# Kernel tuning notes

Hardware: AMD Instinct MI355X
Metric: run time of the kernel (lower is better)

Reference implementation:

```python
import jax, jax.numpy as jnp
import numpy as np

B, S, D, E, K = 4, 4096, 4096, 64, 8


def setup_inputs() -> dict:
    key = jax.random.key(0)
    k1, k2, k3, k4 = jax.random.split(key, 4)
    scale = 1.0 / np.sqrt(D)
    return {
        "mh_output": jax.random.normal(k1, (B, S, D), dtype=jnp.float32),
        "W_route": jax.random.normal(k2, (E, D), dtype=jnp.float32) * scale,
        "b_route": jnp.zeros((E,), dtype=jnp.float32),
        "W_noise": jax.random.normal(k3, (E, D), dtype=jnp.float32) * scale,
        "b_noise": jnp.zeros((E,), dtype=jnp.float32),
        "noise_eps": jax.random.normal(k4, (B, S, E), dtype=jnp.float32),
        "top_k": K,
    }


def reference(mh_output, W_route, b_route, W_noise, b_noise, noise_eps, top_k):
    # two skinny GEMMs: [B,S,D] x [D,E] -> [B,S,E]
    logits = jnp.einsum("bsd,ed->bse", mh_output, W_route) + b_route
    noise_logits = jnp.einsum("bsd,ed->bse", mh_output, W_noise) + b_noise
    noisy_logits = logits + noise_eps * jax.nn.softplus(noise_logits)
    # top-k selection per token over the expert dim
    _, indices = jax.lax.top_k(noisy_logits, top_k)  # [B,S,K]
    # scatter top-k logits into a -inf tensor == mask non-topk entries
    mask = jnp.any(jax.nn.one_hot(indices, noisy_logits.shape[-1], dtype=jnp.bool_), axis=-2)  # [B,S,E]
    sparse_logits = jnp.where(mask, noisy_logits, -jnp.inf)
    router_output = jax.nn.softmax(sparse_logits, axis=-1)
    return router_output, indices
```

## Files before the change

### kernel.cpp

```cpp
#include <hip/hip_runtime.h>
#include <math.h>

#define D_DIM 4096
#define E_DIM 64
#define KTOP 8
#define TAU 2e-4f
#define BM 64
#define NTS 64
#define STB 49152
#define NST 3

#define WS_LIST 1024
#define WS_IMG 66560

typedef __attribute__((ext_vector_type(8))) short bf16x8;
typedef __attribute__((ext_vector_type(4))) float f32x4;

#define MFMA(a, b, c) __builtin_amdgcn_mfma_f32_16x16x32_bf16(a, b, c, 0, 0, 0)

typedef const __attribute__((address_space(1))) void gas_void;
typedef __attribute__((address_space(3))) void las_void;
#define GLL16(src, dst) \
    __builtin_amdgcn_global_load_lds((gas_void*)(src), (las_void*)(dst), 16, 0, 0)
#define SCHED_FENCE() __builtin_amdgcn_sched_barrier(0)

__device__ inline void split8(float4 p, float4 q, bf16x8& h8, bf16x8& l8) {
    float xx[8] = {p.x, p.y, p.z, p.w, q.x, q.y, q.z, q.w};
    union { unsigned int w[4]; bf16x8 v; } H, L;
    #pragma unroll
    for (int i = 0; i < 4; ++i) {
        float a = xx[2 * i], b = xx[2 * i + 1];
        unsigned int hw;
        asm("v_cvt_pk_bf16_f32 %0, %1, %2" : "=v"(hw) : "v"(a), "v"(b));
        float ha = __uint_as_float(hw << 16);
        float hb = __uint_as_float(hw & 0xFFFF0000u);
        float ra = a - ha, rb = b - hb;
        unsigned int lw;
        asm("v_cvt_pk_bf16_f32 %0, %1, %2" : "=v"(lw) : "v"(ra), "v"(rb));
        H.w[i] = hw; L.w[i] = lw;
    }
    h8 = H.v; l8 = L.v;
}

__global__ __launch_bounds__(256)
void preconv(const float* __restrict__ Wr, const float* __restrict__ Wn,
             unsigned short* __restrict__ img, unsigned int* __restrict__ cnt)
{
    if (blockIdx.x == 0 && threadIdx.x == 0) *cnt = 0u;
    int t = blockIdx.x * 256 + threadIdx.x;
    int kt = t >> 9, rem = t & 511;
    int koff = rem >> 7, col = rem & 127;
    int k = kt * 32 + koff * 8;
    const float* base = (col < E_DIM) ? (Wr + (size_t)col * D_DIM)
                                      : (Wn + (size_t)(col - E_DIM) * D_DIM);
    float4 x0 = *(const float4*)(base + k);
    float4 x1 = *(const float4*)(base + k + 4);
    bf16x8 h8, l8;
    split8(x0, x1, h8, l8);
    size_t o = (size_t)kt * 8192 + koff * 1024 + col * 8;
    *(bf16x8*)(img + o) = h8;
    *(bf16x8*)(img + o + 4096) = l8;
}

__global__ __launch_bounds__(512)
void router_main(const float* __restrict__ mh,
                 const unsigned short* __restrict__ Wimg,
                 const float* __restrict__ br, const float* __restrict__ bn,
                 const float* __restrict__ eps,
                 float* __restrict__ out_probs, float* __restrict__ out_idx,
                 unsigned int* __restrict__ cnt, int* __restrict__ list)
{
    extern __shared__ char smem[];
    float* zs = (float*)smem;

    const int tid  = threadIdx.x;
    const int lane = tid & 63;
    const int wv   = tid >> 6;
    const int wr   = wv >> 1;
    const int wc   = wv & 1;
    const int tok0 = blockIdx.x * BM;
    const int rloc = lane & 15;
    const int koff = lane >> 4;
    const int row  = wr * 16 + rloc;

    int boff[4];
    #pragma unroll
    for (int fc = 0; fc < 4; ++fc)
        boff[fc] = koff * 1024 + (wc * 64 + fc * 16 + rloc) * 8;

    const int4* gimg = (const int4*)Wimg;
    const float* arow = mh + (size_t)(tok0 + (tid & 63)) * D_DIM;
    const int aq0 = (tid >> 6) * 4;
    const int aq1 = aq0 + 32;

    f32x4 acc[4];
    #pragma unroll
    for (int fc = 0; fc < 4; ++fc) acc[fc] = {0.f, 0.f, 0.f, 0.f};

    auto stage_issue = [&](int t) {
        char* sb = smem + (t % NST) * STB;
        const int4* gB = gimg + (size_t)t * 2048 + tid;
        int4* dB = (int4*)sb + tid;
        GLL16(gB, dB);
        GLL16(gB + 512,  dB + 512);
        GLL16(gB + 1024, dB + 1024);
        GLL16(gB + 1536, dB + 1536);
        int4* dA = (int4*)(sb + 32768) + tid;
        GLL16(arow + t * 64 + aq0, dA);
        GLL16(arow + t * 64 + aq1, dA + 512);
    };

    stage_issue(0);
    SCHED_FENCE();
    stage_issue(1);
    SCHED_FENCE();
    asm volatile("s_waitcnt vmcnt(6)" ::: "memory");
    SCHED_FENCE();
    __builtin_amdgcn_s_barrier();
    SCHED_FENCE();

    for (int kt = 0; kt < NTS; ++kt) {
        if (kt + 2 < NTS) stage_issue(kt + 2);
        SCHED_FENCE();
        {
            const char* sb = smem + (kt % NST) * STB;
            const unsigned short* Bst = (const unsigned short*)sb;
            const char* sa = sb + 32768;
            #pragma unroll
            for (int s = 0; s < 2; ++s) {
                const int kf = s * 8 + 2 * koff;
                float4 f0 = *(const float4*)(sa + (kf * 64 + row) * 16);
                float4 f1 = *(const float4*)(sa + ((kf + 1) * 64 + row) * 16);
                bf16x8 ah, al;
                split8(f0, f1, ah, al);
                const unsigned short* bb = Bst + s * 8192;
                #pragma unroll
                for (int fc = 0; fc < 4; ++fc) {
                    bf16x8 bh = *(const bf16x8*)(bb + boff[fc]);
                    bf16x8 bl = *(const bf16x8*)(bb + 4096 + boff[fc]);
                    acc[fc] = MFMA(ah, bh, acc[fc]);
                    acc[fc] = MFMA(al, bh, acc[fc]);
                    acc[fc] = MFMA(ah, bl, acc[fc]);
                }
            }
        }
        SCHED_FENCE();
        if (kt + 2 < NTS) {
            asm volatile("s_waitcnt vmcnt(6) lgkmcnt(0)" ::: "memory");
        } else {
            asm volatile("s_waitcnt vmcnt(0) lgkmcnt(0)" ::: "memory");
        }
        SCHED_FENCE();
        __builtin_amdgcn_s_barrier();
        SCHED_FENCE();
    }

    #pragma unroll
    for (int fc = 0; fc < 4; ++fc) {
        const int col = wc * 64 + fc * 16 + rloc;
        const float bias = (col < E_DIM) ? br[col] : bn[col - E_DIM];
        #pragma unroll
        for (int rg = 0; rg < 4; ++rg) {
            const int r = wr * 16 + koff * 4 + rg;
            zs[r * 132 + col] = acc[fc][rg] + bias;
        }
    }
    __syncthreads();

    {
        const int t  = tid >> 3;
        const int e0 = (tid & 7) << 3;
        const float* ep = eps + (size_t)(tok0 + t) * E_DIM + e0;
        #pragma unroll
        for (int j = 0; j < 8; ++j) {
            float zr = zs[t * 132 + e0 + j];
            float zn = zs[t * 132 + 64 + e0 + j];
            float sp = fmaxf(zn, 0.f) + log1pf(expf(-fabsf(zn)));
            zs[t * 132 + e0 + j] = zr + ep[j] * sp;
        }
    }
    __syncthreads();

    for (int tk = 0; tk < 8; ++tk) {
        int t = wv * 8 + tk;
        float v0 = zs[t * 132 + lane];
        float v  = v0;
        float m0 = 0.f, denom = 0.f, prev = 0.f, mingap = INFINITY;
        bool selected = false;
        int rankedIdx = 0;
        #pragma unroll
        for (int k = 0; k < KTOP + 1; ++k) {
            float mv = v; int mi = lane;
            #pragma unroll
            for (int off = 32; off > 0; off >>= 1) {
                float ov = __shfl_xor(mv, off);
                int   oi = __shfl_xor(mi, off);
                if (ov > mv || (ov == mv && oi < mi)) { mv = ov; mi = oi; }
            }
            if (k == 0) m0 = mv; else mingap = fminf(mingap, prev - mv);
            prev = mv;
            if (k < KTOP) {
                denom += expf(mv - m0);
                if (lane == mi) { selected = true; v = -INFINITY; }
                if (lane == k) rankedIdx = mi;
            }
        }
        float p = selected ? expf(v0 - m0) / denom : 0.f;
        size_t tg = (size_t)(tok0 + t);
        out_probs[tg * E_DIM + lane] = p;
        if (lane < KTOP) out_idx[tg * KTOP + lane] = (float)rankedIdx;
        if (mingap < TAU && lane == 0) {
            unsigned int wpos = atomicAdd(cnt, 1u);
            list[wpos] = (int)tg;
        }
    }
}

__global__ __launch_bounds__(256)
void refine_fp64(const float* __restrict__ mh,
                 const float* __restrict__ Wr, const float* __restrict__ br,
                 const float* __restrict__ Wn, const float* __restrict__ bn,
                 const float* __restrict__ eps,
                 float* __restrict__ out_probs, float* __restrict__ out_idx,
                 const unsigned int* __restrict__ cnt, const int* __restrict__ list)
{
    __shared__ double red[128];
    const unsigned int n = *cnt;
    const int tid  = threadIdx.x;
    const int lane = tid & 63;
    const int wv   = tid >> 6;

    for (unsigned int i = blockIdx.x; i < n; i += gridDim.x) {
        const int tok = list[i];
        const float* xb = mh + (size_t)tok * D_DIM;

        for (int r = 0; r < 32; ++r) {
            const int rrow = wv * 32 + r;
            const float* wp = (rrow < E_DIM) ? (Wr + (size_t)rrow * D_DIM)
                                             : (Wn + (size_t)(rrow - E_DIM) * D_DIM);
            double s0 = 0.0, s1 = 0.0, s2 = 0.0, s3 = 0.0;
            #pragma unroll 4
            for (int k = lane * 4; k < D_DIM; k += 256) {
                float4 xv = *(const float4*)(xb + k);
                float4 w4 = *(const float4*)(wp + k);
                s0 += (double)xv.x * (double)w4.x;
                s1 += (double)xv.y * (double)w4.y;
                s2 += (double)xv.z * (double)w4.z;
                s3 += (double)xv.w * (double)w4.w;
            }
            double s = (s0 + s1) + (s2 + s3);
            #pragma unroll
            for (int off = 32; off > 0; off >>= 1) s += __shfl_xor(s, off);
            if (lane == 0) red[rrow] = s;
        }
        __syncthreads();

        if (wv == 0) {
            double zr = red[lane] + (double)br[lane];
            double zn = red[E_DIM + lane] + (double)bn[lane];
            double sp = fmax(zn, 0.0) + log1p(exp(-fabs(zn)));
            double nl = zr + (double)eps[(size_t)tok * E_DIM + lane] * sp;
            double v = nl, m0 = 0.0, denom = 0.0;
            bool selected = false;
            int rankedIdx = 0;
            #pragma unroll
            for (int k = 0; k < KTOP; ++k) {
                double mv = v; int mi = lane;
                #pragma unroll
                for (int off = 32; off > 0; off >>= 1) {
                    double ov = __shfl_xor(mv, off);
                    int    oi = __shfl_xor(mi, off);
                    if (ov > mv || (ov == mv && oi < mi)) { mv = ov; mi = oi; }
                }
                if (k == 0) m0 = mv;
                denom += exp(mv - m0);
                if (lane == mi) { selected = true; v = -INFINITY; }
                if (lane == k) rankedIdx = mi;
            }
            float p = selected ? (float)(exp(nl - m0) / denom) : 0.f;
            out_probs[(size_t)tok * E_DIM + lane] = p;
            if (lane < KTOP) out_idx[(size_t)tok * KTOP + lane] = (float)rankedIdx;
        }
        __syncthreads();
    }
}

extern "C" void kernel_launch(void* const* d_in, const int* in_sizes, int n_in,
                              void* d_out, int out_size, void* d_ws, size_t ws_size,
                              hipStream_t stream) {
    const float* mh  = (const float*)d_in[0];
    const float* Wr  = (const float*)d_in[1];
    const float* br  = (const float*)d_in[2];
    const float* Wn  = (const float*)d_in[3];
    const float* bn  = (const float*)d_in[4];
    const float* eps = (const float*)d_in[5];

    const int ntok = in_sizes[0] / D_DIM;
    float* out_probs = (float*)d_out;
    float* out_idx   = (float*)d_out + (size_t)ntok * E_DIM;

    unsigned int* cnt = (unsigned int*)d_ws;
    int* list = (int*)((char*)d_ws + WS_LIST);
    unsigned short* img = (unsigned short*)((char*)d_ws + WS_IMG);

    hipLaunchKernelGGL(preconv, dim3(256), dim3(256), 0, stream, Wr, Wn, img, cnt);
    hipLaunchKernelGGL(router_main, dim3(ntok / BM), dim3(512), NST * STB, stream,
                       mh, img, br, bn, eps, out_probs, out_idx, cnt, list);
    hipLaunchKernelGGL(refine_fp64, dim3(1024), dim3(256), 0, stream,
                       mh, Wr, br, Wn, bn, eps, out_probs, out_idx, cnt, list);
}
```

Baseline: 232.6 us.

## Split fused router kernel into separate GEMM and epilogue kernels

The fused GEMM+top-k kernel becomes two kernels. The first writes raw fp32 logits for both the route and noise projections to a workspace buffer. The second applies the biases, softplus noise, top-k and softmax, using smaller 256-thread blocks of 32 tokens. This frees the GEMM kernel from the serial per-token epilogue tail and its LDS reuse. In exchange it adds a global round-trip of the logit buffer and one more kernel launch.

After: 232.3 us. About the same (-0.1%).

```diff
diff --git a/kernel.cpp b/kernel.cpp
--- a/kernel.cpp
+++ b/kernel.cpp
@@ -12,6 +12,7 @@
 
 #define WS_LIST 1024
 #define WS_IMG 66560
+#define WS_Z   (WS_IMG + 2097152)
 
 typedef __attribute__((ext_vector_type(8))) short bf16x8;
 typedef __attribute__((ext_vector_type(4))) float f32x4;
@@ -63,15 +64,11 @@
 }
 
 __global__ __launch_bounds__(512)
-void router_main(const float* __restrict__ mh,
-                 const unsigned short* __restrict__ Wimg,
-                 const float* __restrict__ br, const float* __restrict__ bn,
-                 const float* __restrict__ eps,
-                 float* __restrict__ out_probs, float* __restrict__ out_idx,
-                 unsigned int* __restrict__ cnt, int* __restrict__ list)
+void gemm_k(const float* __restrict__ mh,
+            const unsigned short* __restrict__ Wimg,
+            float* __restrict__ zbuf)
 {
     extern __shared__ char smem[];
-    float* zs = (float*)smem;
 
     const int tid  = threadIdx.x;
     const int lane = tid & 63;
@@ -155,15 +152,36 @@
         SCHED_FENCE();
     }
 
+    float* zb = zbuf + (size_t)tok0 * 128;
     #pragma unroll
     for (int fc = 0; fc < 4; ++fc) {
         const int col = wc * 64 + fc * 16 + rloc;
-        const float bias = (col < E_DIM) ? br[col] : bn[col - E_DIM];
         #pragma unroll
         for (int rg = 0; rg < 4; ++rg) {
             const int r = wr * 16 + koff * 4 + rg;
-            zs[r * 132 + col] = acc[fc][rg] + bias;
-        }
+            zb[r * 128 + col] = acc[fc][rg];
+        }
+    }
+}
+
+__global__ __launch_bounds__(256)
+void epi_k(const float* __restrict__ zbuf,
+           const float* __restrict__ br, const float* __restrict__ bn,
+           const float* __restrict__ eps,
+           float* __restrict__ out_probs, float* __restrict__ out_idx,
+           unsigned int* __restrict__ cnt, int* __restrict__ list)
+{
+    __shared__ float zs[32 * 132];
+    const int tid  = threadIdx.x;
+    const int lane = tid & 63;
+    const int wv   = tid >> 6;
+    const int tok0 = blockIdx.x * 32;
+
+    for (int i = tid; i < 1024; i += 256) {
+        int t = i >> 5, q = i & 31;
+        float4 v = *(const float4*)(zbuf + (size_t)(tok0 + t) * 128 + q * 4);
+        int b = t * 132 + q * 4;
+        zs[b] = v.x; zs[b + 1] = v.y; zs[b + 2] = v.z; zs[b + 3] = v.w;
     }
     __syncthreads();
 
@@ -173,8 +191,8 @@
         const float* ep = eps + (size_t)(tok0 + t) * E_DIM + e0;
         #pragma unroll
         for (int j = 0; j < 8; ++j) {
-            float zr = zs[t * 132 + e0 + j];
-            float zn = zs[t * 132 + 64 + e0 + j];
+            float zr = zs[t * 132 + e0 + j] + br[e0 + j];
+            float zn = zs[t * 132 + 64 + e0 + j] + bn[e0 + j];
             float sp = fmaxf(zn, 0.f) + log1pf(expf(-fabsf(zn)));
             zs[t * 132 + e0 + j] = zr + ep[j] * sp;
         }
@@ -302,10 +320,13 @@
     unsigned int* cnt = (unsigned int*)d_ws;
     int* list = (int*)((char*)d_ws + WS_LIST);
     unsigned short* img = (unsigned short*)((char*)d_ws + WS_IMG);
+    float* zbuf = (float*)((char*)d_ws + WS_Z);
 
     hipLaunchKernelGGL(preconv, dim3(256), dim3(256), 0, stream, Wr, Wn, img, cnt);
-    hipLaunchKernelGGL(router_main, dim3(ntok / BM), dim3(512), NST * STB, stream,
-                       mh, img, br, bn, eps, out_probs, out_idx, cnt, list);
+    hipLaunchKernelGGL(gemm_k, dim3(ntok / BM), dim3(512), NST * STB, stream,
+                       mh, img, zbuf);
+    hipLaunchKernelGGL(epi_k, dim3(ntok / 32), dim3(256), 0, stream,
+                       zbuf, br, bn, eps, out_probs, out_idx, cnt, list);
     hipLaunchKernelGGL(refine_fp64, dim3(1024), dim3(256), 0, stream,
                        mh, Wr, br, Wn, bn, eps, out_probs, out_idx, cnt, list);
 }
```
